# Kernel tuning notes

Hardware: AMD Instinct MI355X
Metric: run time of the kernel (lower is better)

The kernel has to match this reference:

```python
import jax, jax.numpy as jnp
import numpy as np

VOCAB = 50257
EMBED = 512
HIDDEN = 1024
UNITS = HIDDEN // 2  # per-direction LSTM units
B, S, T = 32, 8, 128


def _lstm_bias(units):
    # Keras unit_forget_bias=True: bias = [0 (i), 1 (f), 0 (c), 0 (o)]
    return jnp.concatenate([jnp.zeros((units,)), jnp.ones((units,)),
                            jnp.zeros((2 * units,))])


def setup_inputs() -> dict:
    key = jax.random.key(0)
    ks = jax.random.split(key, 8)
    # token ids with variable-length zero padding (pad_token_id=0)
    x = jax.random.randint(ks[0], (B, S, T), 1, VOCAB)
    lengths = jax.random.randint(ks[1], (B, S, 1), T // 2, T + 1)
    pos = jnp.arange(T)[None, None, :]
    x = jnp.where(pos < lengths, x, 0).astype(jnp.int32)

    emb_table = jax.random.normal(ks[2], (VOCAB, EMBED), jnp.float32) * 0.05

    def glorot(k, shape):
        fan = np.sqrt(2.0 / (shape[0] + shape[1]))
        return jax.random.normal(k, shape, jnp.float32) * fan

    W_f = glorot(ks[3], (EMBED, 4 * UNITS))
    U_f = glorot(ks[4], (UNITS, 4 * UNITS))
    W_b = glorot(ks[5], (EMBED, 4 * UNITS))
    U_b = glorot(ks[6], (UNITS, 4 * UNITS))
    b_f = _lstm_bias(UNITS)
    b_b = _lstm_bias(UNITS)
    return {"x": x, "emb_table": emb_table,
            "W_f": W_f, "U_f": U_f, "b_f": b_f,
            "W_b": W_b, "U_b": U_b, "b_b": b_b}


def _masked_lstm_final(xW, mask, U):
    """xW: (N, T, 4u) precomputed input projections (+bias); mask: (N, T) bool.
    Returns final hidden state (N, u) with Keras masking semantics: masked
    timesteps are skipped (state held)."""
    N = xW.shape[0]
    u = U.shape[0]
    h0 = jnp.zeros((N, u), xW.dtype)
    c0 = jnp.zeros((N, u), xW.dtype)

    def step(carry, inp):
        h, c = carry
        z, m = inp  # z: (N, 4u), m: (N,)
        z = z + h @ U
        i, f, g, o = jnp.split(z, 4, axis=-1)
        i = jax.nn.sigmoid(i)
        f = jax.nn.sigmoid(f)
        g = jnp.tanh(g)
        o = jax.nn.sigmoid(o)
        c_new = f * c + i * g
        h_new = o * jnp.tanh(c_new)
        m = m[:, None]
        return (jnp.where(m, h_new, h), jnp.where(m, c_new, c)), None

    (hT, _), _ = jax.lax.scan(
        step, (h0, c0),
        (jnp.swapaxes(xW, 0, 1), jnp.swapaxes(mask, 0, 1)))
    return hT


def reference(x, emb_table, W_f, U_f, b_f, W_b, U_b, b_b):
    Bx, Sx, Tx = x.shape
    N = Bx * Sx
    ids = x.reshape(N, Tx)
    mask = ids != 0  # mask_zero=True
    emb = emb_table[ids]  # (N, T, E)

    # forward direction
    xWf = emb @ W_f + b_f  # (N, T, 4u), one big GEMM up front
    h_fwd = _masked_lstm_final(xWf, mask, U_f)

    # backward direction: reverse time and mask (Keras go_backwards)
    emb_rev = emb[:, ::-1, :]
    mask_rev = mask[:, ::-1]
    xWb = emb_rev @ W_b + b_b
    h_bwd = _masked_lstm_final(xWb, mask_rev, U_b)

    out = jnp.concatenate([h_fwd, h_bwd], axis=-1)  # (N, hidden_dim)
    return out.reshape(Bx, Sx, HIDDEN)
```

## Files before the change

kernel.cpp:

```cpp
#include <hip/hip_runtime.h>

typedef _Float16 half_t;
typedef _Float16 half8 __attribute__((ext_vector_type(8)));
typedef float floatx4 __attribute__((ext_vector_type(4)));

#define NSEQ   256
#define TLEN   128
#define EMBD   512
#define UNITSZ 512
#define GC     2048
#define NTOK   32768
#define NCOL   4096
#define KDIM   512

constexpr size_t OFF_EMB = 0;
constexpr size_t OFF_WT  = 33554432;
constexpr size_t OFF_UT  = OFF_WT + 4194304;
constexpr size_t OFF_HB  = OFF_UT + 4194304;
constexpr size_t OFF_CNT = OFF_HB + 1048576;
constexpr size_t OFF_MSK = OFF_CNT + 4096;
constexpr size_t OFF_XW  = OFF_MSK + 4096;

__device__ inline float sigm(float x)  { return 1.0f / (1.0f + __expf(-x)); }
__device__ inline float tanhx(float x) { return 2.0f / (1.0f + __expf(-2.0f * x)) - 1.0f; }

__device__ inline unsigned ld_flag(const unsigned* p) {
    unsigned v;
    asm volatile("global_load_dword %0, %1, off sc0 sc1\n\t"
                 "s_waitcnt vmcnt(0)" : "=v"(v) : "v"(p) : "memory");
    return v;
}

__device__ inline void st_flag(unsigned* p, unsigned v) {
    asm volatile("global_store_dword %0, %1, off sc0 sc1" :: "v"(p), "v"(v) : "memory");
}

__device__ inline void st_h(unsigned short* p, unsigned v) {
    asm volatile("global_store_short %0, %1, off sc0 sc1" :: "v"(p), "v"(v) : "memory");
}

__device__ inline void af_issue(const half_t* ap, half8* af) {
    asm volatile(
        "global_load_dwordx4 %0, %16, off sc0 sc1\n\t"
        "global_load_dwordx4 %1, %16, off offset:64 sc0 sc1\n\t"
        "global_load_dwordx4 %2, %16, off offset:128 sc0 sc1\n\t"
        "global_load_dwordx4 %3, %16, off offset:192 sc0 sc1\n\t"
        "global_load_dwordx4 %4, %16, off offset:256 sc0 sc1\n\t"
        "global_load_dwordx4 %5, %16, off offset:320 sc0 sc1\n\t"
        "global_load_dwordx4 %6, %16, off offset:384 sc0 sc1\n\t"
        "global_load_dwordx4 %7, %16, off offset:448 sc0 sc1\n\t"
        "global_load_dwordx4 %8, %16, off offset:512 sc0 sc1\n\t"
        "global_load_dwordx4 %9, %16, off offset:576 sc0 sc1\n\t"
        "global_load_dwordx4 %10, %16, off offset:640 sc0 sc1\n\t"
        "global_load_dwordx4 %11, %16, off offset:704 sc0 sc1\n\t"
        "global_load_dwordx4 %12, %16, off offset:768 sc0 sc1\n\t"
        "global_load_dwordx4 %13, %16, off offset:832 sc0 sc1\n\t"
        "global_load_dwordx4 %14, %16, off offset:896 sc0 sc1\n\t"
        "global_load_dwordx4 %15, %16, off offset:960 sc0 sc1"
        : "=&v"(af[0]), "=&v"(af[1]), "=&v"(af[2]), "=&v"(af[3]),
          "=&v"(af[4]), "=&v"(af[5]), "=&v"(af[6]), "=&v"(af[7]),
          "=&v"(af[8]), "=&v"(af[9]), "=&v"(af[10]), "=&v"(af[11]),
          "=&v"(af[12]), "=&v"(af[13]), "=&v"(af[14]), "=&v"(af[15])
        : "v"(ap) : "memory");
}

__device__ inline void xv_issue(const half_t* p0, const half_t* p1,
                                const half_t* p2, const half_t* p3,
                                unsigned* xvr) {
    asm volatile(
        "global_load_ushort %0, %16, off\n\t"
        "global_load_ushort %1, %16, off offset:1024\n\t"
        "global_load_ushort %2, %16, off offset:2048\n\t"
        "global_load_ushort %3, %16, off offset:3072\n\t"
        "global_load_ushort %4, %17, off\n\t"
        "global_load_ushort %5, %17, off offset:1024\n\t"
        "global_load_ushort %6, %17, off offset:2048\n\t"
        "global_load_ushort %7, %17, off offset:3072\n\t"
        "global_load_ushort %8, %18, off\n\t"
        "global_load_ushort %9, %18, off offset:1024\n\t"
        "global_load_ushort %10, %18, off offset:2048\n\t"
        "global_load_ushort %11, %18, off offset:3072\n\t"
        "global_load_ushort %12, %19, off\n\t"
        "global_load_ushort %13, %19, off offset:1024\n\t"
        "global_load_ushort %14, %19, off offset:2048\n\t"
        "global_load_ushort %15, %19, off offset:3072"
        : "=&v"(xvr[0]), "=&v"(xvr[1]), "=&v"(xvr[2]), "=&v"(xvr[3]),
          "=&v"(xvr[4]), "=&v"(xvr[5]), "=&v"(xvr[6]), "=&v"(xvr[7]),
          "=&v"(xvr[8]), "=&v"(xvr[9]), "=&v"(xvr[10]), "=&v"(xvr[11]),
          "=&v"(xvr[12]), "=&v"(xvr[13]), "=&v"(xvr[14]), "=&v"(xvr[15])
        : "v"(p0), "v"(p1), "v"(p2), "v"(p3) : "memory");
}

__global__ void pack_kernel(const float* __restrict__ Wf, const float* __restrict__ Uf,
                            const float* __restrict__ Wb, const float* __restrict__ Ub,
                            half_t* __restrict__ WT, half_t* __restrict__ UT) {
    int c = blockIdx.x * 256 + threadIdx.x;
    int arr = c >> 18;
    int r = c & 262143;
    int kc = r >> 12;
    int gc = r & 4095;
    int dir = gc >> 11;
    int g = gc & 2047;
    const float* src = (arr == 0) ? (dir ? Wb : Wf) : (dir ? Ub : Uf);
    half_t* dst = (arr == 0) ? WT : UT;
    half8 v;
#pragma unroll
    for (int j = 0; j < 8; ++j)
        v[j] = (half_t)src[(size_t)(kc * 8 + j) * GC + g];
    *(half8*)(dst + (size_t)gc * KDIM + kc * 8) = v;
}

__global__ void zero_kernel(unsigned* __restrict__ hb_and_cnt) {
    int i = blockIdx.x * 256 + threadIdx.x;
    if (i < 263168) hb_and_cnt[i] = 0u;
}

__global__ void mask_kernel(const int* __restrict__ x, unsigned long long* __restrict__ mk) {
    int n = blockIdx.x;
    int l = threadIdx.x;
    unsigned long long b0 = __ballot(x[n * TLEN + l] != 0);
    unsigned long long b1 = __ballot(x[n * TLEN + 64 + l] != 0);
    if (l == 0) { mk[n * 2] = b0; mk[n * 2 + 1] = b1; }
}

__global__ void gather_kernel(const int* __restrict__ x, const float* __restrict__ tab,
                              half_t* __restrict__ embf) {
    int g = blockIdx.x * 256 + threadIdx.x;
    int token = g >> 6;
    int k = (g & 63) * 8;
    int id = x[token];
    const float* s = tab + (size_t)id * EMBD + k;
    float4 a = *(const float4*)(s);
    float4 b = *(const float4*)(s + 4);
    half8 v;
    v[0] = (half_t)a.x; v[1] = (half_t)a.y; v[2] = (half_t)a.z; v[3] = (half_t)a.w;
    v[4] = (half_t)b.x; v[5] = (half_t)b.y; v[6] = (half_t)b.z; v[7] = (half_t)b.w;
    *(half8*)(embf + (size_t)token * EMBD + k) = v;
}

__global__ __launch_bounds__(256, 2) void gemm_kernel(const half_t* __restrict__ embf,
                                                      const half_t* __restrict__ WT,
                                                      const float* __restrict__ bf,
                                                      const float* __restrict__ bb,
                                                      half_t* __restrict__ xw) {
    __shared__ half_t As[128 * 40];
    __shared__ half_t Bs[128 * 40];
    int bx = blockIdx.x;
    int bm = bx & 255, bn = bx >> 8;
    int r0 = bm * 128, c0 = bn * 128;
    int tid = threadIdx.x;
    int w = tid >> 6, l = tid & 63;
    int q = l >> 4, cl = l & 15;
    int mq = (w >> 1) * 64, nq = (w & 1) * 64;

    floatx4 acc[4][4];
#pragma unroll
    for (int a = 0; a < 4; ++a)
#pragma unroll
        for (int b = 0; b < 4; ++b) acc[a][b] = (floatx4){0.f, 0.f, 0.f, 0.f};

    for (int kb = 0; kb < 16; ++kb) {
#pragma unroll
        for (int cc = 0; cc < 2; ++cc) {
            int c = tid + cc * 256;
            int row = c >> 2, qt = c & 3;
            half8 va = *(const half8*)(embf + (size_t)(r0 + row) * KDIM + kb * 32 + qt * 8);
            *(half8*)(As + row * 40 + qt * 8) = va;
            half8 vb = *(const half8*)(WT + (size_t)(c0 + row) * KDIM + kb * 32 + qt * 8);
            *(half8*)(Bs + row * 40 + qt * 8) = vb;
        }
        __syncthreads();
        half8 af[4], bfr[4];
#pragma unroll
        for (int mb = 0; mb < 4; ++mb)
            af[mb] = *(const half8*)(As + (mq + mb * 16 + cl) * 40 + q * 8);
#pragma unroll
        for (int nb = 0; nb < 4; ++nb)
            bfr[nb] = *(const half8*)(Bs + (nq + nb * 16 + cl) * 40 + q * 8);
#pragma unroll
        for (int mb = 0; mb < 4; ++mb)
#pragma unroll
            for (int nb = 0; nb < 4; ++nb)
                acc[mb][nb] = __builtin_amdgcn_mfma_f32_16x16x32_f16(af[mb], bfr[nb], acc[mb][nb], 0, 0, 0);
        __syncthreads();
    }
#pragma unroll
    for (int nb = 0; nb < 4; ++nb) {
        int col = c0 + nq + nb * 16 + cl;
        int dir = col >> 11, gcol = col & 2047;
        float bias = dir ? bb[gcol] : bf[gcol];
#pragma unroll
        for (int mb = 0; mb < 4; ++mb) {
#pragma unroll
            for (int r = 0; r < 4; ++r) {
                int row = r0 + mq + mb * 16 + q * 4 + r;
                xw[(size_t)row * NCOL + col] = (half_t)(acc[mb][nb][r] + bias);
            }
        }
    }
}

__global__ __launch_bounds__(256, 1) void lstm_kernel(const half_t* __restrict__ xw,
                                                      const half_t* __restrict__ UT,
                                                      half_t* __restrict__ hbuf,
                                                      const unsigned long long* __restrict__ mk,
                                                      float* __restrict__ out,
                                                      unsigned* __restrict__ cnt) {
    int bx = blockIdx.x;
    int grp = bx & 31;
    int wgc = bx >> 5;
    int dir = grp >> 4;
    int rowg = grp & 15;
    int tid = threadIdx.x;
    int w = tid >> 6, l = tid & 63;
    int q = l >> 4, cl = l & 15;
    int cg = wgc * 4 + w;
    int ub = cg * 16;
    int r0 = rowg * 16;
    int wid = wgc * 4 + w;

    half8 bfrag[64];
#pragma unroll
    for (int kk = 0; kk < 16; ++kk)
#pragma unroll
        for (int cf = 0; cf < 4; ++cf)
            bfrag[kk * 4 + cf] = *(const half8*)(UT + (size_t)(dir * 2048 + cf * 512 + ub + cl) * KDIM + kk * 32 + q * 8);

    unsigned long long mlo[4], mhi[4];
#pragma unroll
    for (int r = 0; r < 4; ++r) {
        int n = r0 + q * 4 + r;
        mlo[r] = mk[n * 2];
        mhi[r] = mk[n * 2 + 1];
    }

    float cs[4] = {0.f, 0.f, 0.f, 0.f};
    float hs[4] = {0.f, 0.f, 0.f, 0.f};
    unsigned* flg = cnt + grp * 32;
    unsigned* fpoll = flg + (l & 31);
    int colb = dir * 2048 + ub + cl;

    const half_t* ap0 = hbuf + (size_t)(dir * 2 + 0) * NSEQ * UNITSZ + (size_t)(r0 + cl) * UNITSZ + q * 8;
    const half_t* ap1 = ap0 + (size_t)NSEQ * UNITSZ;
    half_t* hw0 = hbuf + (size_t)(dir * 2 + 0) * NSEQ * UNITSZ + (size_t)(r0 + q * 4) * UNITSZ + ub + cl;
    half_t* hw1 = hw0 + (size_t)NSEQ * UNITSZ;

    const half_t* xb0 = xw + (size_t)(r0 + q * 4 + 0) * TLEN * NCOL + colb;
    const half_t* xb1 = xw + (size_t)(r0 + q * 4 + 1) * TLEN * NCOL + colb;
    const half_t* xb2 = xw + (size_t)(r0 + q * 4 + 2) * TLEN * NCOL + colb;
    const half_t* xb3 = xw + (size_t)(r0 + q * 4 + 3) * TLEN * NCOL + colb;

    unsigned xvr[16];
    {
        int tI = dir ? 127 : 0;
        xv_issue(xb0 + (size_t)tI * NCOL, xb1 + (size_t)tI * NCOL,
                 xb2 + (size_t)tI * NCOL, xb3 + (size_t)tI * NCOL, xvr);
    }
    asm volatile("s_waitcnt vmcnt(0)" ::: "memory");
    __builtin_amdgcn_sched_barrier(0);

#pragma unroll 1
    for (int t = 0; t < TLEN; ++t) {
        int tIdx = dir ? (127 - t) : t;
        int rpar = t & 1;
        half8 af[16];
        if (t > 0) {
            unsigned tgt = (unsigned)t;
            for (unsigned sp = 0;; ++sp) {
                unsigned v = ld_flag(fpoll);
                if (__all((int)(v >= tgt))) break;
                if (sp >= (1u << 20)) break;
                __builtin_amdgcn_s_sleep(1);
            }
            af_issue(rpar ? ap1 : ap0, af);
        }
        floatx4 a0, a1, a2, a3;
#pragma unroll
        for (int r = 0; r < 4; ++r) {
            a0[r] = (float)__builtin_bit_cast(half_t, (unsigned short)xvr[r * 4 + 0]);
            a1[r] = (float)__builtin_bit_cast(half_t, (unsigned short)xvr[r * 4 + 1]);
            a2[r] = (float)__builtin_bit_cast(half_t, (unsigned short)xvr[r * 4 + 2]);
            a3[r] = (float)__builtin_bit_cast(half_t, (unsigned short)xvr[r * 4 + 3]);
        }
        if (t > 0) {
            asm volatile("s_waitcnt vmcnt(0)" ::: "memory");
            __builtin_amdgcn_sched_barrier(0);
#pragma unroll
            for (int kk = 0; kk < 16; ++kk) {
                a0 = __builtin_amdgcn_mfma_f32_16x16x32_f16(af[kk], bfrag[kk * 4 + 0], a0, 0, 0, 0);
                a1 = __builtin_amdgcn_mfma_f32_16x16x32_f16(af[kk], bfrag[kk * 4 + 1], a1, 0, 0, 0);
                a2 = __builtin_amdgcn_mfma_f32_16x16x32_f16(af[kk], bfrag[kk * 4 + 2], a2, 0, 0, 0);
                a3 = __builtin_amdgcn_mfma_f32_16x16x32_f16(af[kk], bfrag[kk * 4 + 3], a3, 0, 0, 0);
            }
        }
        unsigned short* hdst = (unsigned short*)(rpar ? hw0 : hw1);
#pragma unroll
        for (int r = 0; r < 4; ++r) {
            unsigned long long mw = (tIdx & 64) ? mhi[r] : mlo[r];
            bool keep = (mw >> (tIdx & 63)) & 1ull;
            float iv = sigm(a0[r]);
            float fv = sigm(a1[r]);
            float gv = tanhx(a2[r]);
            float ov = sigm(a3[r]);
            float cn = fv * cs[r] + iv * gv;
            float hn = ov * tanhx(cn);
            if (keep) { cs[r] = cn; hs[r] = hn; }
            unsigned hv = (unsigned)__builtin_bit_cast(unsigned short, (half_t)hs[r]);
            st_h(hdst + r * 512, hv);
        }
        asm volatile("s_waitcnt vmcnt(0)" ::: "memory");
        __builtin_amdgcn_sched_barrier(0);
        if (l == 0)
            st_flag(flg + wid, (unsigned)(t + 1));
        if (t + 1 < TLEN) {
            int tN = dir ? (126 - t) : (t + 1);
            xv_issue(xb0 + (size_t)tN * NCOL, xb1 + (size_t)tN * NCOL,
                     xb2 + (size_t)tN * NCOL, xb3 + (size_t)tN * NCOL, xvr);
        }
    }
#pragma unroll
    for (int r = 0; r < 4; ++r) {
        int n = r0 + q * 4 + r;
        out[(size_t)n * 1024 + dir * 512 + ub + cl] = hs[r];
    }
}

extern "C" void kernel_launch(void* const* d_in, const int* in_sizes, int n_in,
                              void* d_out, int out_size, void* d_ws, size_t ws_size,
                              hipStream_t stream) {
    const int*   x    = (const int*)d_in[0];
    const float* tab  = (const float*)d_in[1];
    const float* Wf   = (const float*)d_in[2];
    const float* Uf   = (const float*)d_in[3];
    const float* bf   = (const float*)d_in[4];
    const float* Wb   = (const float*)d_in[5];
    const float* Ub   = (const float*)d_in[6];
    const float* bb   = (const float*)d_in[7];
    float* out = (float*)d_out;

    char* ws = (char*)d_ws;
    half_t*   embf = (half_t*)(ws + OFF_EMB);
    half_t*   WT   = (half_t*)(ws + OFF_WT);
    half_t*   UT   = (half_t*)(ws + OFF_UT);
    half_t*   hbuf = (half_t*)(ws + OFF_HB);
    unsigned* cnt  = (unsigned*)(ws + OFF_CNT);
    unsigned long long* mkb = (unsigned long long*)(ws + OFF_MSK);
    half_t*   xw   = (half_t*)(ws + OFF_XW);
    unsigned* hbz  = (unsigned*)(ws + OFF_HB);

    pack_kernel<<<2048, 256, 0, stream>>>(Wf, Uf, Wb, Ub, WT, UT);
    zero_kernel<<<1028, 256, 0, stream>>>(hbz);
    mask_kernel<<<256, 64, 0, stream>>>(x, mkb);
    gather_kernel<<<8192, 256, 0, stream>>>(x, tab, embf);
    gemm_kernel<<<8192, 256, 0, stream>>>(embf, WT, bf, bb, xw);
    lstm_kernel<<<256, 256, 0, stream>>>(xw, UT, hbuf, mkb, out, cnt);
}
```

Measured before the change: 1.188 ms.

## Replace per-step flag barrier with timestep-tagged hidden-state words

Each hidden value is now stored as a 32-bit word holding the fp16 value plus the timestep tag in the upper half. Consumers poll the data directly until every tag matches, in two halves, so the second half's load overlaps the first half's MFMAs. This removes the separate flag store, its store-drain wait, and the flag poll round trip from the recurrent critical path. The cost is twice the hidden-state traffic and retry loads. The tagged buffer reuses the embedding workspace, which is zeroed after the GEMM.

```diff
diff --git a/kernel.cpp b/kernel.cpp
--- a/kernel.cpp
+++ b/kernel.cpp
@@ -24,44 +24,61 @@
 __device__ inline float sigm(float x)  { return 1.0f / (1.0f + __expf(-x)); }
 __device__ inline float tanhx(float x) { return 2.0f / (1.0f + __expf(-2.0f * x)) - 1.0f; }
 
-__device__ inline unsigned ld_flag(const unsigned* p) {
+__device__ inline unsigned ld_probe(const unsigned* p) {
     unsigned v;
     asm volatile("global_load_dword %0, %1, off sc0 sc1\n\t"
                  "s_waitcnt vmcnt(0)" : "=v"(v) : "v"(p) : "memory");
     return v;
 }
 
-__device__ inline void st_flag(unsigned* p, unsigned v) {
+__device__ inline void st_tag(unsigned* p, unsigned v) {
     asm volatile("global_store_dword %0, %1, off sc0 sc1" :: "v"(p), "v"(v) : "memory");
 }
 
-__device__ inline void st_h(unsigned short* p, unsigned v) {
-    asm volatile("global_store_short %0, %1, off sc0 sc1" :: "v"(p), "v"(v) : "memory");
-}
-
-__device__ inline void af_issue(const half_t* ap, half8* af) {
+__device__ inline void hb_batch(const unsigned* p, uint4* d) {
     asm volatile(
         "global_load_dwordx4 %0, %16, off sc0 sc1\n\t"
-        "global_load_dwordx4 %1, %16, off offset:64 sc0 sc1\n\t"
+        "global_load_dwordx4 %1, %16, off offset:16 sc0 sc1\n\t"
         "global_load_dwordx4 %2, %16, off offset:128 sc0 sc1\n\t"
-        "global_load_dwordx4 %3, %16, off offset:192 sc0 sc1\n\t"
+        "global_load_dwordx4 %3, %16, off offset:144 sc0 sc1\n\t"
         "global_load_dwordx4 %4, %16, off offset:256 sc0 sc1\n\t"
-        "global_load_dwordx4 %5, %16, off offset:320 sc0 sc1\n\t"
+        "global_load_dwordx4 %5, %16, off offset:272 sc0 sc1\n\t"
         "global_load_dwordx4 %6, %16, off offset:384 sc0 sc1\n\t"
-        "global_load_dwordx4 %7, %16, off offset:448 sc0 sc1\n\t"
+        "global_load_dwordx4 %7, %16, off offset:400 sc0 sc1\n\t"
         "global_load_dwordx4 %8, %16, off offset:512 sc0 sc1\n\t"
-        "global_load_dwordx4 %9, %16, off offset:576 sc0 sc1\n\t"
+        "global_load_dwordx4 %9, %16, off offset:528 sc0 sc1\n\t"
         "global_load_dwordx4 %10, %16, off offset:640 sc0 sc1\n\t"
-        "global_load_dwordx4 %11, %16, off offset:704 sc0 sc1\n\t"
+        "global_load_dwordx4 %11, %16, off offset:656 sc0 sc1\n\t"
         "global_load_dwordx4 %12, %16, off offset:768 sc0 sc1\n\t"
-        "global_load_dwordx4 %13, %16, off offset:832 sc0 sc1\n\t"
+        "global_load_dwordx4 %13, %16, off offset:784 sc0 sc1\n\t"
         "global_load_dwordx4 %14, %16, off offset:896 sc0 sc1\n\t"
-        "global_load_dwordx4 %15, %16, off offset:960 sc0 sc1"
-        : "=&v"(af[0]), "=&v"(af[1]), "=&v"(af[2]), "=&v"(af[3]),
-          "=&v"(af[4]), "=&v"(af[5]), "=&v"(af[6]), "=&v"(af[7]),
-          "=&v"(af[8]), "=&v"(af[9]), "=&v"(af[10]), "=&v"(af[11]),
-          "=&v"(af[12]), "=&v"(af[13]), "=&v"(af[14]), "=&v"(af[15])
-        : "v"(ap) : "memory");
+        "global_load_dwordx4 %15, %16, off offset:912 sc0 sc1"
+        : "=&v"(d[0]), "=&v"(d[1]), "=&v"(d[2]), "=&v"(d[3]),
+          "=&v"(d[4]), "=&v"(d[5]), "=&v"(d[6]), "=&v"(d[7]),
+          "=&v"(d[8]), "=&v"(d[9]), "=&v"(d[10]), "=&v"(d[11]),
+          "=&v"(d[12]), "=&v"(d[13]), "=&v"(d[14]), "=&v"(d[15])
+        : "v"(p) : "memory");
+}
+
+__device__ inline unsigned minscan16(const uint4* d) {
+    unsigned m = 0xffffffffu;
+#pragma unroll
+    for (int i = 0; i < 16; ++i) {
+        m = m < d[i].x ? m : d[i].x;
+        m = m < d[i].y ? m : d[i].y;
+        m = m < d[i].z ? m : d[i].z;
+        m = m < d[i].w ? m : d[i].w;
+    }
+    return m;
+}
+
+__device__ inline half8 unpack8(const uint4& a, const uint4& b) {
+    union { unsigned u[4]; half8 v; } c;
+    c.u[0] = (a.x & 0xffffu) | (a.y << 16);
+    c.u[1] = (a.z & 0xffffu) | (a.w << 16);
+    c.u[2] = (b.x & 0xffffu) | (b.y << 16);
+    c.u[3] = (b.z & 0xffffu) | (b.w << 16);
+    return c.v;
 }
 
 __device__ inline void xv_issue(const half_t* p0, const half_t* p1,
@@ -110,9 +127,8 @@
     *(half8*)(dst + (size_t)gc * KDIM + kc * 8) = v;
 }
 
-__global__ void zero_kernel(unsigned* __restrict__ hb_and_cnt) {
-    int i = blockIdx.x * 256 + threadIdx.x;
-    if (i < 263168) hb_and_cnt[i] = 0u;
+__global__ void zero32_kernel(unsigned* __restrict__ p) {
+    p[blockIdx.x * 256 + threadIdx.x] = 0u;
 }
 
 __global__ void mask_kernel(const int* __restrict__ x, unsigned long long* __restrict__ mk) {
@@ -202,10 +218,9 @@
 
 __global__ __launch_bounds__(256, 1) void lstm_kernel(const half_t* __restrict__ xw,
                                                       const half_t* __restrict__ UT,
-                                                      half_t* __restrict__ hbuf,
+                                                      unsigned* __restrict__ hb,
                                                       const unsigned long long* __restrict__ mk,
-                                                      float* __restrict__ out,
-                                                      unsigned* __restrict__ cnt) {
+                                                      float* __restrict__ out) {
     int bx = blockIdx.x;
     int grp = bx & 31;
     int wgc = bx >> 5;
@@ -217,7 +232,6 @@
     int cg = wgc * 4 + w;
     int ub = cg * 16;
     int r0 = rowg * 16;
-    int wid = wgc * 4 + w;
 
     half8 bfrag[64];
 #pragma unroll
@@ -236,14 +250,16 @@
 
     float cs[4] = {0.f, 0.f, 0.f, 0.f};
     float hs[4] = {0.f, 0.f, 0.f, 0.f};
-    unsigned* flg = cnt + grp * 32;
-    unsigned* fpoll = flg + (l & 31);
     int colb = dir * 2048 + ub + cl;
 
-    const half_t* ap0 = hbuf + (size_t)(dir * 2 + 0) * NSEQ * UNITSZ + (size_t)(r0 + cl) * UNITSZ + q * 8;
-    const half_t* ap1 = ap0 + (size_t)NSEQ * UNITSZ;
-    half_t* hw0 = hbuf + (size_t)(dir * 2 + 0) * NSEQ * UNITSZ + (size_t)(r0 + q * 4) * UNITSZ + ub + cl;
-    half_t* hw1 = hw0 + (size_t)NSEQ * UNITSZ;
+    unsigned* hbd = hb + (size_t)(dir * 2) * NSEQ * UNITSZ;
+    const unsigned* ap0 = hbd + (size_t)(r0 + cl) * UNITSZ + q * 8;
+    const unsigned* ap1 = ap0 + (size_t)NSEQ * UNITSZ;
+    unsigned* hw0 = hbd + (size_t)(r0 + q * 4) * UNITSZ + ub + cl;
+    unsigned* hw1 = hw0 + (size_t)NSEQ * UNITSZ;
+    int jb = l & 7, wwp = (l >> 3) & 3, rr = (l >> 5) * 8;
+    const unsigned* pp0 = hbd + (size_t)(r0 + rr) * UNITSZ + jb * 64 + wwp * 16;
+    const unsigned* pp1 = pp0 + (size_t)NSEQ * UNITSZ;
 
     const half_t* xb0 = xw + (size_t)(r0 + q * 4 + 0) * TLEN * NCOL + colb;
     const half_t* xb1 = xw + (size_t)(r0 + q * 4 + 1) * TLEN * NCOL + colb;
@@ -263,37 +279,77 @@
     for (int t = 0; t < TLEN; ++t) {
         int tIdx = dir ? (127 - t) : t;
         int rpar = t & 1;
-        half8 af[16];
+        floatx4 a0, a1, a2, a3;
         if (t > 0) {
-            unsigned tgt = (unsigned)t;
+            unsigned tg = (unsigned)t;
+            const unsigned* pp = rpar ? pp1 : pp0;
             for (unsigned sp = 0;; ++sp) {
-                unsigned v = ld_flag(fpoll);
-                if (__all((int)(v >= tgt))) break;
+                unsigned pv = ld_probe(pp);
+                if (__all((int)((pv >> 16) == tg))) break;
                 if (sp >= (1u << 20)) break;
                 __builtin_amdgcn_s_sleep(1);
             }
-            af_issue(rpar ? ap1 : ap0, af);
-        }
-        floatx4 a0, a1, a2, a3;
-#pragma unroll
-        for (int r = 0; r < 4; ++r) {
-            a0[r] = (float)__builtin_bit_cast(half_t, (unsigned short)xvr[r * 4 + 0]);
-            a1[r] = (float)__builtin_bit_cast(half_t, (unsigned short)xvr[r * 4 + 1]);
-            a2[r] = (float)__builtin_bit_cast(half_t, (unsigned short)xvr[r * 4 + 2]);
-            a3[r] = (float)__builtin_bit_cast(half_t, (unsigned short)xvr[r * 4 + 3]);
-        }
-        if (t > 0) {
-            asm volatile("s_waitcnt vmcnt(0)" ::: "memory");
-            __builtin_amdgcn_sched_barrier(0);
-#pragma unroll
-            for (int kk = 0; kk < 16; ++kk) {
+            const unsigned* bp = rpar ? ap1 : ap0;
+            uint4 d0[16];
+            for (unsigned sp = 0;; ++sp) {
+                hb_batch(bp, d0);
+                asm volatile("s_waitcnt vmcnt(0)" ::: "memory");
+                __builtin_amdgcn_sched_barrier(0);
+                unsigned m = minscan16(d0);
+                if (__all((int)((m >> 16) == tg))) break;
+                if (sp >= 65536u) break;
+            }
+            half8 af[16];
+#pragma unroll
+            for (int kk = 0; kk < 8; ++kk)
+                af[kk] = unpack8(d0[2 * kk], d0[2 * kk + 1]);
+            uint4 d1[16];
+            hb_batch(bp + 256, d1);
+#pragma unroll
+            for (int r = 0; r < 4; ++r) {
+                a0[r] = (float)__builtin_bit_cast(half_t, (unsigned short)xvr[r * 4 + 0]);
+                a1[r] = (float)__builtin_bit_cast(half_t, (unsigned short)xvr[r * 4 + 1]);
+                a2[r] = (float)__builtin_bit_cast(half_t, (unsigned short)xvr[r * 4 + 2]);
+                a3[r] = (float)__builtin_bit_cast(half_t, (unsigned short)xvr[r * 4 + 3]);
+            }
+#pragma unroll
+            for (int kk = 0; kk < 8; ++kk) {
                 a0 = __builtin_amdgcn_mfma_f32_16x16x32_f16(af[kk], bfrag[kk * 4 + 0], a0, 0, 0, 0);
                 a1 = __builtin_amdgcn_mfma_f32_16x16x32_f16(af[kk], bfrag[kk * 4 + 1], a1, 0, 0, 0);
                 a2 = __builtin_amdgcn_mfma_f32_16x16x32_f16(af[kk], bfrag[kk * 4 + 2], a2, 0, 0, 0);
                 a3 = __builtin_amdgcn_mfma_f32_16x16x32_f16(af[kk], bfrag[kk * 4 + 3], a3, 0, 0, 0);
             }
+            asm volatile("s_waitcnt vmcnt(0)" ::: "memory");
+            __builtin_amdgcn_sched_barrier(0);
+            for (unsigned sp = 0;; ++sp) {
+                unsigned m = minscan16(d1);
+                if (__all((int)((m >> 16) == tg))) break;
+                if (sp >= 65536u) break;
+                hb_batch(bp + 256, d1);
+                asm volatile("s_waitcnt vmcnt(0)" ::: "memory");
+                __builtin_amdgcn_sched_barrier(0);
+            }
+#pragma unroll
+            for (int kk = 8; kk < 16; ++kk)
+                af[kk] = unpack8(d1[2 * (kk - 8)], d1[2 * (kk - 8) + 1]);
+#pragma unroll
+            for (int kk = 8; kk < 16; ++kk) {
+                a0 = __builtin_amdgcn_mfma_f32_16x16x32_f16(af[kk], bfrag[kk * 4 + 0], a0, 0, 0, 0);
+                a1 = __builtin_amdgcn_mfma_f32_16x16x32_f16(af[kk], bfrag[kk * 4 + 1], a1, 0, 0, 0);
+                a2 = __builtin_amdgcn_mfma_f32_16x16x32_f16(af[kk], bfrag[kk * 4 + 2], a2, 0, 0, 0);
+                a3 = __builtin_amdgcn_mfma_f32_16x16x32_f16(af[kk], bfrag[kk * 4 + 3], a3, 0, 0, 0);
+            }
+        } else {
+#pragma unroll
+            for (int r = 0; r < 4; ++r) {
+                a0[r] = (float)__builtin_bit_cast(half_t, (unsigned short)xvr[r * 4 + 0]);
+                a1[r] = (float)__builtin_bit_cast(half_t, (unsigned short)xvr[r * 4 + 1]);
+                a2[r] = (float)__builtin_bit_cast(half_t, (unsigned short)xvr[r * 4 + 2]);
+                a3[r] = (float)__builtin_bit_cast(half_t, (unsigned short)xvr[r * 4 + 3]);
+            }
         }
-        unsigned short* hdst = (unsigned short*)(rpar ? hw0 : hw1);
+        unsigned* hdst = rpar ? hw0 : hw1;
+        unsigned tagv = ((unsigned)(t + 1)) << 16;
 #pragma unroll
         for (int r = 0; r < 4; ++r) {
             unsigned long long mw = (tIdx & 64) ? mhi[r] : mlo[r];
@@ -305,18 +361,16 @@
             float cn = fv * cs[r] + iv * gv;
             float hn = ov * tanhx(cn);
             if (keep) { cs[r] = cn; hs[r] = hn; }
-            unsigned hv = (unsigned)__builtin_bit_cast(unsigned short, (half_t)hs[r]);
-            st_h(hdst + r * 512, hv);
+            unsigned hv = tagv | (unsigned)__builtin_bit_cast(unsigned short, (half_t)hs[r]);
+            st_tag(hdst + r * 512, hv);
         }
-        asm volatile("s_waitcnt vmcnt(0)" ::: "memory");
-        __builtin_amdgcn_sched_barrier(0);
-        if (l == 0)
-            st_flag(flg + wid, (unsigned)(t + 1));
         if (t + 1 < TLEN) {
             int tN = dir ? (126 - t) : (t + 1);
             xv_issue(xb0 + (size_t)tN * NCOL, xb1 + (size_t)tN * NCOL,
                      xb2 + (size_t)tN * NCOL, xb3 + (size_t)tN * NCOL, xvr);
         }
+        asm volatile("s_waitcnt vmcnt(0)" ::: "memory");
+        __builtin_amdgcn_sched_barrier(0);
     }
 #pragma unroll
     for (int r = 0; r < 4; ++r) {
@@ -342,16 +396,14 @@
     half_t*   embf = (half_t*)(ws + OFF_EMB);
     half_t*   WT   = (half_t*)(ws + OFF_WT);
     half_t*   UT   = (half_t*)(ws + OFF_UT);
-    half_t*   hbuf = (half_t*)(ws + OFF_HB);
-    unsigned* cnt  = (unsigned*)(ws + OFF_CNT);
+    unsigned* hb32 = (unsigned*)(ws + OFF_EMB);
     unsigned long long* mkb = (unsigned long long*)(ws + OFF_MSK);
     half_t*   xw   = (half_t*)(ws + OFF_XW);
-    unsigned* hbz  = (unsigned*)(ws + OFF_HB);
 
     pack_kernel<<<2048, 256, 0, stream>>>(Wf, Uf, Wb, Ub, WT, UT);
-    zero_kernel<<<1028, 256, 0, stream>>>(hbz);
     mask_kernel<<<256, 64, 0, stream>>>(x, mkb);
     gather_kernel<<<8192, 256, 0, stream>>>(x, tab, embf);
     gemm_kernel<<<8192, 256, 0, stream>>>(embf, WT, bf, bb, xw);
-    lstm_kernel<<<256, 256, 0, stream>>>(xw, UT, hbuf, mkb, out, cnt);
-}
+    zero32_kernel<<<2048, 256, 0, stream>>>(hb32);
+    lstm_kernel<<<256, 256, 0, stream>>>(xw, UT, hb32, mkb, out);
+}
```

Result: slower. 1.329 ms (+11.9%).
